# Optimization experiments

Hardware: AMD Instinct MI355X
Metric: run time of the kernel (lower is better)

Reference implementation:

```python
import jax, jax.numpy as jnp
import numpy as np

B, N, D, H = 4, 2048, 1024, 16
DH = D // H  # head dim = 64


def positional_encoding(n, dim):
    # Faithful vectorization of the numpy double loop in PositionalEncoding.
    i = jnp.arange(dim)
    even_i = (i % 2) == 0
    denom_i = 10000.0 ** (2.0 * jnp.where(even_i, i, i - 1).astype(jnp.float32) / dim)
    pos = jnp.arange(n, dtype=jnp.float32)[:, None]  # [n,1]
    base = jnp.where(even_i[None, :], jnp.sin(pos / denom_i), jnp.cos(pos / denom_i))  # [n,dim]
    p = jnp.arange(n)
    even_p = (p % 2) == 0
    denom_p = 10000.0 ** (2.0 * jnp.where(even_p, p, p - 1).astype(jnp.float32) / n)  # [n]
    j = jnp.arange(dim, dtype=jnp.float32)[None, :]  # [1,dim]
    mult = jnp.where(even_p[:, None], jnp.sin(j / denom_p[:, None]), jnp.cos(j / denom_p[:, None]))  # [n,dim]
    return base * mult


def setup_inputs() -> dict:
    key = jax.random.key(0)
    ks = jax.random.split(key, 4)
    s = 1.0 / np.sqrt(D)
    return {
        "data": jax.random.normal(ks[0], (B, N, D), dtype=jnp.float32),
        "Wq": jax.random.normal(ks[1], (D, D), dtype=jnp.float32) * s,
        "bq": jnp.zeros((D,), dtype=jnp.float32),
        "Wk": jax.random.normal(ks[2], (D, D), dtype=jnp.float32) * s,
        "bk": jnp.zeros((D,), dtype=jnp.float32),
        "Wv": jax.random.normal(ks[3], (D, D), dtype=jnp.float32) * s,
        "bv": jnp.zeros((D,), dtype=jnp.float32),
    }


def _split_heads(x):
    # tf.concat(tf.split(x, H, axis=-1), axis=0): head-major [H*B, N, DH]
    b, n, d = x.shape
    return x.reshape(b, n, H, DH).transpose(2, 0, 1, 3).reshape(H * b, n, DH)


def reference(data, Wq, bq, Wk, bk, Wv, bv):
    b, n, d = data.shape
    x = data + positional_encoding(n, d).astype(data.dtype)  # [B,N,D]
    q = _split_heads(x @ Wq + bq)  # [H*B,N,DH]
    k = _split_heads(x @ Wk + bk)
    v = _split_heads(x @ Wv + bv)
    # scale uses last dim of key AFTER split, i.e. head_dim
    scores = jnp.einsum('bqd,bkd->bqk', q, k) / jnp.sqrt(jnp.float32(DH))  # [H*B,N,N]
    w = jax.nn.softmax(scores, axis=-1)
    return jnp.einsum('bqk,bkd->bqd', w, v)  # [H*B,N,DH]
```

## Files before the change

kernel.cpp:

```cpp
#include <hip/hip_runtime.h>
#include <hip/hip_bf16.h>

#define BB 4
#define NN 2048
#define DD 1024
#define HH 16
#define DHH 64
#define HB (HH*BB)

typedef __bf16 bf16;
typedef __bf16 bf16x4v __attribute__((ext_vector_type(4)));
typedef __bf16 bf16x8 __attribute__((ext_vector_type(8)));
typedef float f32x4 __attribute__((ext_vector_type(4)));
typedef float f32x16 __attribute__((ext_vector_type(16)));
typedef unsigned u32x2 __attribute__((ext_vector_type(2)));

#if __has_builtin(__builtin_amdgcn_permlane32_swap)
#define HAVE_PLSWAP 1
#else
#define HAVE_PLSWAP 0
#endif

#define QSCALE 0.18033688011112042f

__device__ __forceinline__ void async16(const void* g, void* l) {
    __builtin_amdgcn_global_load_lds(
        (const __attribute__((address_space(1))) unsigned int*)g,
        (__attribute__((address_space(3))) unsigned int*)l, 16, 0, 0);
}

__device__ __forceinline__ unsigned pkbf(float a, float b) {
    union { bf16 h[2]; unsigned u; } x;
    x.h[0] = (bf16)a; x.h[1] = (bf16)b;
    return x.u;
}

__global__ void pe_add_kernel(const float* __restrict__ data, bf16* __restrict__ xb) {
    int t = blockIdx.x * blockDim.x + threadIdx.x;
    int base = t * 4;
    int row = base >> 10;
    int d0 = base & 1023;
    int n = row & (NN - 1);
    const float LOG2_10000 = 13.287712379549449f;
    int pn = n & ~1;
    float denom_p = __builtin_amdgcn_exp2f((2.0f * (float)pn / (float)NN) * LOG2_10000);
    bool even_p = (n & 1) == 0;
    float4 dv = *(const float4*)(data + base);
    float din[4] = {dv.x, dv.y, dv.z, dv.w};
    bf16x4v ov;
    #pragma unroll
    for (int u = 0; u < 4; ++u) {
        int d = d0 + u;
        int di = d & ~1;
        float denom_i = __builtin_amdgcn_exp2f((2.0f * (float)di / (float)DD) * LOG2_10000);
        float a = (float)n / denom_i;
        float basev = ((d & 1) == 0) ? __sinf(a) : __cosf(a);
        float bm = (float)d / denom_p;
        float mult = even_p ? __sinf(bm) : __cosf(bm);
        ov[u] = (bf16)(din[u] + basev * mult);
    }
    *(bf16x4v*)(xb + base) = ov;
}

__global__ void wtrans_kernel(const float* __restrict__ Wq, const float* __restrict__ Wk,
                              const float* __restrict__ Wv, bf16* __restrict__ Bw) {
    const float* W = (blockIdx.z == 0) ? Wq : (blockIdx.z == 1) ? Wk : Wv;
    bf16* Wt = Bw + (size_t)blockIdx.z * 1024 * 1024;
    __shared__ float s[32][33];
    int bx = blockIdx.x * 32;
    int by = blockIdx.y * 32;
    int tx = threadIdx.x, ty = threadIdx.y;
    #pragma unroll
    for (int i = 0; i < 32; i += 8)
        s[ty + i][tx] = W[(by + ty + i) * DD + bx + tx];
    __syncthreads();
    #pragma unroll
    for (int i = 0; i < 32; i += 8)
        Wt[(size_t)(bx + ty + i) * DD + by + tx] = (bf16)s[tx][ty + i];
}

__launch_bounds__(256)
__global__ void gemm_qkv_fused(const bf16* __restrict__ A,
                               const bf16* __restrict__ Bw,
                               const float* __restrict__ bq, const float* __restrict__ bk,
                               const float* __restrict__ bv,
                               bf16* __restrict__ Qs, bf16* __restrict__ Ks,
                               bf16* __restrict__ Vb) {
    __shared__ char smem[36864];
    int tid = threadIdx.x;
    int w = tid >> 6, lane = tid & 63, l32 = lane & 31, hi = lane >> 5;
    int bi = blockIdx.x;
    int bn = bi >> 6;
    int bm = (bi & 7) * 8 + ((bi >> 3) & 7);
    int m0 = bm * 128, n0 = bn * 128;
    int wm = (w & 1) * 64, wn = (w >> 1) * 64;

    int srow = tid >> 2;
    int g4 = (tid & 3) ^ (srow & 3);
    const bf16* aS0 = A + (size_t)(m0 + srow) * DD + g4 * 8;
    const bf16* aS1 = aS0 + (size_t)64 * DD;
    const bf16* bS0 = Bw + (size_t)(n0 + srow) * DD + g4 * 8;
    const bf16* bS1 = bS0 + (size_t)64 * DD;

    f32x16 acc[2][2];
    #pragma unroll
    for (int i = 0; i < 2; ++i)
        #pragma unroll
        for (int j = 0; j < 2; ++j)
            #pragma unroll
            for (int r = 0; r < 16; ++r) acc[i][j][r] = 0.f;

    async16(aS0, smem + w * 1024);
    async16(aS1, smem + 4096 + w * 1024);
    async16(bS0, smem + 8192 + w * 1024);
    async16(bS1, smem + 12288 + w * 1024);
    __syncthreads();

    for (int kk = 0; kk < DD; kk += 32) {
        char* buf  = smem + ((kk >> 5) & 1) * 16384;
        char* nbuf = smem + (((kk >> 5) & 1) ^ 1) * 16384;
        if (kk + 32 < DD) {
            async16(aS0 + kk + 32, nbuf + w * 1024);
            async16(aS1 + kk + 32, nbuf + 4096 + w * 1024);
            async16(bS0 + kk + 32, nbuf + 8192 + w * 1024);
            async16(bS1 + kk + 32, nbuf + 12288 + w * 1024);
        }
        const char* As = buf;
        const char* Bs = buf + 8192;
        bf16x8 af[2][2], bfr[2][2];
        #pragma unroll
        for (int mt = 0; mt < 2; ++mt) {
            int row = wm + mt * 32 + l32;
            #pragma unroll
            for (int kc = 0; kc < 2; ++kc)
                af[mt][kc] = *(const bf16x8*)(As + row * 64 + ((kc * 2 + hi) ^ (l32 & 3)) * 16);
        }
        #pragma unroll
        for (int nt = 0; nt < 2; ++nt) {
            int row = wn + nt * 32 + l32;
            #pragma unroll
            for (int kc = 0; kc < 2; ++kc)
                bfr[nt][kc] = *(const bf16x8*)(Bs + row * 64 + ((kc * 2 + hi) ^ (l32 & 3)) * 16);
        }
        #pragma unroll
        for (int mt = 0; mt < 2; ++mt)
            #pragma unroll
            for (int nt = 0; nt < 2; ++nt)
                #pragma unroll
                for (int kc = 0; kc < 2; ++kc)
                    acc[mt][nt] = __builtin_amdgcn_mfma_f32_32x32x16_bf16(
                        af[mt][kc], bfr[nt][kc], acc[mt][nt], 0, 0, 0);
        __syncthreads();
    }

    int mat = n0 >> 10;
    if (mat < 2) {
        const float* bias_p = (mat == 0) ? bq : bk;
        #pragma unroll
        for (int nt = 0; nt < 2; ++nt) {
            int ncol = (n0 + wn + nt * 32 + l32) & 1023;
            float bias = bias_p[ncol];
            int h = ncol >> 6, dh = ncol & 63;
            #pragma unroll
            for (int mt = 0; mt < 2; ++mt) {
                int rowbase = m0 + wm + mt * 32 + 4 * hi;
                #pragma unroll
                for (int m4 = 0; m4 < 4; ++m4) {
                    #pragma unroll
                    for (int rr = 0; rr < 4; ++rr) {
                        int mrow = rowbase + 8 * m4 + rr;
                        int b_ = mrow >> 11, nn_ = mrow & 2047;
                        int hbi = h * BB + b_;
                        float v = acc[mt][nt][m4 * 4 + rr] + bias;
                        if (mat == 0)
                            Qs[((size_t)hbi * NN + nn_) * DHH + dh] = (bf16)(v * QSCALE);
                        else
                            Ks[((size_t)hbi * NN + nn_) * DHH + dh] = (bf16)v;
                    }
                }
            }
        }
    } else {
        bf16* vl = (bf16*)smem;
        #pragma unroll
        for (int nt = 0; nt < 2; ++nt) {
            int ncol_l = wn + nt * 32 + l32;
            float bias = bv[(n0 + ncol_l) & 1023];
            #pragma unroll
            for (int mt = 0; mt < 2; ++mt) {
                int m_base = wm + mt * 32 + 4 * hi;
                #pragma unroll
                for (int m4 = 0; m4 < 4; ++m4) {
                    bf16x4v q;
                    #pragma unroll
                    for (int rr = 0; rr < 4; ++rr)
                        q[rr] = (bf16)(acc[mt][nt][m4 * 4 + rr] + bias);
                    *(bf16x4v*)(vl + ncol_l * 130 + m_base + 8 * m4) = q;
                }
            }
        }
        __syncthreads();
        int b_ = m0 >> 11, nn0 = m0 & 2047;
        #pragma unroll
        for (int p = 0; p < 2; ++p) {
            int ncol = p * 64 + (tid >> 2);
            int ncg = (n0 + ncol) & 1023;
            int h = ncg >> 6, dh = ncg & 63;
            bf16* dst = Vb + ((size_t)(h * BB + b_) * DHH + dh) * NN + nn0;
            #pragma unroll
            for (int i = 0; i < 4; ++i) {
                int eoff = ((tid & 3) + 4 * i) * 8;
                bf16x8 vv = *(const bf16x8*)(vl + ncol * 130 + eoff);
                *(bf16x8*)(dst + eoff) = vv;
            }
        }
    }
}

__launch_bounds__(256, 4)
__global__ void attn_kernel(const bf16* __restrict__ Qs,
                            const bf16* __restrict__ Ks,
                            const bf16* __restrict__ Vb,
                            float* __restrict__ out) {
    __shared__ char smem[32768];
    int tid = threadIdx.x;
    int w = tid >> 6, lane = tid & 63, l32 = lane & 31, hi = lane >> 5;
    int bi = blockIdx.x;
    int xcd = bi & 7, j = bi >> 3;
    int hb = xcd * 8 + (j & 7);
    int qb = j >> 3;
    int q0 = qb * 128 + w * 32;

    const bf16* qbase = Qs + ((size_t)hb * NN + q0 + l32) * DHH + hi * 8;
    bf16x8 qf[4];
    #pragma unroll
    for (int c = 0; c < 4; ++c)
        qf[c] = *(const bf16x8*)(qbase + c * 16);

    int srow = tid >> 3;
    int g8 = (tid & 7) ^ (srow & 7);
    const bf16* ksrc = Ks + ((size_t)hb * NN + srow) * DHH + g8 * 8;
    const bf16* vsrc = Vb + ((size_t)hb * DHH + srow) * NN + g8 * 8;

    f32x16 o[2], lacc;
    #pragma unroll
    for (int d = 0; d < 2; ++d)
        #pragma unroll
        for (int r = 0; r < 16; ++r) o[d][r] = 0.f;
    #pragma unroll
    for (int r = 0; r < 16; ++r) lacc[r] = 0.f;
    const bf16x8 onesf = {(bf16)1.f, (bf16)1.f, (bf16)1.f, (bf16)1.f,
                          (bf16)1.f, (bf16)1.f, (bf16)1.f, (bf16)1.f};

    async16(ksrc,            smem + w * 1024);
    async16(ksrc + 32 * 64,  smem + 4096 + w * 1024);
    async16(vsrc,            smem + 8192 + w * 1024);
    async16(vsrc + 32 * NN,  smem + 12288 + w * 1024);
    __syncthreads();

    for (int kt = 0; kt < NN; kt += 64) {
        char* buf  = smem + ((kt >> 6) & 1) * 16384;
        char* nbuf = smem + (((kt >> 6) & 1) ^ 1) * 16384;
        if (kt + 64 < NN) {
            async16(ksrc + (size_t)(kt + 64) * 64,      nbuf + w * 1024);
            async16(ksrc + (size_t)(kt + 96) * 64,      nbuf + 4096 + w * 1024);
            async16(vsrc + (kt + 64),                   nbuf + 8192 + w * 1024);
            async16(vsrc + (size_t)32 * NN + (kt + 64), nbuf + 12288 + w * 1024);
        }
        const char* ktile = buf;
        const char* vtile = buf + 8192;

        f32x16 sa[2];
        #pragma unroll
        for (int t = 0; t < 2; ++t) {
            #pragma unroll
            for (int r = 0; r < 16; ++r) sa[t][r] = 0.f;
            int row = t * 32 + l32;
            #pragma unroll
            for (int c = 0; c < 4; ++c) {
                bf16x8 kf = *(const bf16x8*)(ktile + row * 128 + ((c * 2 + hi) ^ (l32 & 7)) * 16);
                sa[t] = __builtin_amdgcn_mfma_f32_32x32x16_bf16(kf, qf[c], sa[t], 0, 0, 0);
            }
        }

        unsigned dw[2][4][2];
        #pragma unroll
        for (int t = 0; t < 2; ++t) {
            #pragma unroll
            for (int m4 = 0; m4 < 4; ++m4) {
                float p0 = __builtin_amdgcn_exp2f(sa[t][m4 * 4 + 0]);
                float p1 = __builtin_amdgcn_exp2f(sa[t][m4 * 4 + 1]);
                float p2 = __builtin_amdgcn_exp2f(sa[t][m4 * 4 + 2]);
                float p3 = __builtin_amdgcn_exp2f(sa[t][m4 * 4 + 3]);
                dw[t][m4][0] = pkbf(p0, p1);
                dw[t][m4][1] = pkbf(p2, p3);
            }
        }

        #pragma unroll
        for (int c = 0; c < 4; ++c) {
            int t = c >> 1, mlo = (c & 1) * 2;
            unsigned a0 = dw[t][mlo][0],     a1 = dw[t][mlo][1];
            unsigned b0 = dw[t][mlo + 1][0], b1 = dw[t][mlo + 1][1];
            union { unsigned u[4]; bf16x8 v; } pu;
#if HAVE_PLSWAP
            u32x2 r0 = __builtin_amdgcn_permlane32_swap(a0, b0, false, false);
            u32x2 r1 = __builtin_amdgcn_permlane32_swap(a1, b1, false, false);
            pu.u[0] = r0.x; pu.u[1] = r1.x; pu.u[2] = r0.y; pu.u[3] = r1.y;
#else
            unsigned own0 = hi ? b0 : a0, own1 = hi ? b1 : a1;
            unsigned snd0 = hi ? a0 : b0, snd1 = hi ? a1 : b1;
            unsigned rcv0 = __shfl_xor(snd0, 32, 64);
            unsigned rcv1 = __shfl_xor(snd1, 32, 64);
            pu.u[0] = hi ? rcv0 : own0;
            pu.u[1] = hi ? rcv1 : own1;
            pu.u[2] = hi ? own0 : rcv0;
            pu.u[3] = hi ? own1 : rcv1;
#endif
            #pragma unroll
            for (int d = 0; d < 2; ++d) {
                int row = d * 32 + l32;
                bf16x8 vf = *(const bf16x8*)(vtile + row * 128 + ((c * 2 + hi) ^ (l32 & 7)) * 16);
                o[d] = __builtin_amdgcn_mfma_f32_32x32x16_bf16(vf, pu.v, o[d], 0, 0, 0);
            }
            lacc = __builtin_amdgcn_mfma_f32_32x32x16_bf16(onesf, pu.v, lacc, 0, 0, 0);
        }
        __syncthreads();
    }

    float inv = 1.0f / lacc[0];
    float* ob = out + ((size_t)hb * NN + q0 + l32) * DHH + 4 * hi;
    #pragma unroll
    for (int d = 0; d < 2; ++d) {
        #pragma unroll
        for (int m4 = 0; m4 < 4; ++m4) {
            f32x4 vv;
            vv[0] = o[d][m4 * 4 + 0] * inv;
            vv[1] = o[d][m4 * 4 + 1] * inv;
            vv[2] = o[d][m4 * 4 + 2] * inv;
            vv[3] = o[d][m4 * 4 + 3] * inv;
            *(f32x4*)(ob + d * 32 + 8 * m4) = vv;
        }
    }
}

extern "C" void kernel_launch(void* const* d_in, const int* in_sizes, int n_in,
                              void* d_out, int out_size, void* d_ws, size_t ws_size,
                              hipStream_t stream) {
    const float* data = (const float*)d_in[0];
    const float* Wq   = (const float*)d_in[1];
    const float* bq   = (const float*)d_in[2];
    const float* Wk   = (const float*)d_in[3];
    const float* bk   = (const float*)d_in[4];
    const float* Wv   = (const float*)d_in[5];
    const float* bv   = (const float*)d_in[6];
    float* out = (float*)d_out;

    char* ws = (char*)d_ws;
    bf16* xb = (bf16*)ws; ws += (size_t)8192 * 1024 * 2;
    bf16* Bw = (bf16*)ws; ws += (size_t)3072 * 1024 * 2;
    bf16* Qs = (bf16*)ws; ws += (size_t)HB * NN * DHH * 2;
    bf16* Ks = (bf16*)ws; ws += (size_t)HB * NN * DHH * 2;
    bf16* Vb = (bf16*)ws; ws += (size_t)HB * NN * DHH * 2;

    pe_add_kernel<<<8192, 256, 0, stream>>>(data, xb);
    dim3 tb(32, 8), tg(32, 32, 3);
    wtrans_kernel<<<tg, tb, 0, stream>>>(Wq, Wk, Wv, Bw);
    gemm_qkv_fused<<<1536, 256, 0, stream>>>(xb, Bw, bq, bk, bv, Qs, Ks, Vb);
    attn_kernel<<<1024, 256, 0, stream>>>(Qs, Ks, Vb, out);
}
```

Before: 260.4 us.

## Split attention waves across query and key halves, reduce partial outputs in LDS

```diff
diff --git a/kernel.cpp b/kernel.cpp
--- a/kernel.cpp
+++ b/kernel.cpp
@@ -217,40 +217,43 @@
     }
 }
 
-__launch_bounds__(256, 4)
+__launch_bounds__(256, 3)
 __global__ void attn_kernel(const bf16* __restrict__ Qs,
                             const bf16* __restrict__ Ks,
                             const bf16* __restrict__ Vb,
                             float* __restrict__ out) {
-    __shared__ char smem[32768];
+    __shared__ char smem[33280];
     int tid = threadIdx.x;
     int w = tid >> 6, lane = tid & 63, l32 = lane & 31, hi = lane >> 5;
+    int qh = w & 1, kh = w >> 1;
     int bi = blockIdx.x;
-    int xcd = bi & 7, j = bi >> 3;
-    int hb = xcd * 8 + (j & 7);
-    int qb = j >> 3;
-    int q0 = qb * 128 + w * 32;
-
-    const bf16* qbase = Qs + ((size_t)hb * NN + q0 + l32) * DHH + hi * 8;
-    bf16x8 qf[4];
-    #pragma unroll
-    for (int c = 0; c < 4; ++c)
-        qf[c] = *(const bf16x8*)(qbase + c * 16);
+    int xcd = bi & 7, jj = bi >> 3;
+    int hb = xcd * 8 + (jj & 7);
+    int qb = jj >> 3;
+    int q0 = qb * 128;
+
+    bf16x8 qf[2][4];
+    #pragma unroll
+    for (int qs = 0; qs < 2; ++qs) {
+        const bf16* qbase = Qs + ((size_t)hb * NN + q0 + qh * 64 + qs * 32 + l32) * DHH + hi * 8;
+        #pragma unroll
+        for (int c = 0; c < 4; ++c)
+            qf[qs][c] = *(const bf16x8*)(qbase + c * 16);
+    }
 
     int srow = tid >> 3;
     int g8 = (tid & 7) ^ (srow & 7);
     const bf16* ksrc = Ks + ((size_t)hb * NN + srow) * DHH + g8 * 8;
     const bf16* vsrc = Vb + ((size_t)hb * DHH + srow) * NN + g8 * 8;
 
-    f32x16 o[2], lacc;
-    #pragma unroll
-    for (int d = 0; d < 2; ++d)
-        #pragma unroll
-        for (int r = 0; r < 16; ++r) o[d][r] = 0.f;
-    #pragma unroll
-    for (int r = 0; r < 16; ++r) lacc[r] = 0.f;
-    const bf16x8 onesf = {(bf16)1.f, (bf16)1.f, (bf16)1.f, (bf16)1.f,
-                          (bf16)1.f, (bf16)1.f, (bf16)1.f, (bf16)1.f};
+    f32x16 o[2][2];
+    #pragma unroll
+    for (int qs = 0; qs < 2; ++qs)
+        #pragma unroll
+        for (int d = 0; d < 2; ++d)
+            #pragma unroll
+            for (int r = 0; r < 16; ++r) o[qs][d][r] = 0.f;
+    float ts[2] = {0.f, 0.f};
 
     async16(ksrc,            smem + w * 1024);
     async16(ksrc + 32 * 64,  smem + 4096 + w * 1024);
@@ -270,77 +273,135 @@
         const char* ktile = buf;
         const char* vtile = buf + 8192;
 
+        bf16x8 kf[4];
+        int krow = kh * 32 + l32;
+        #pragma unroll
+        for (int c = 0; c < 4; ++c)
+            kf[c] = *(const bf16x8*)(ktile + krow * 128 + ((c * 2 + hi) ^ (l32 & 7)) * 16);
+
         f32x16 sa[2];
         #pragma unroll
-        for (int t = 0; t < 2; ++t) {
-            #pragma unroll
-            for (int r = 0; r < 16; ++r) sa[t][r] = 0.f;
-            int row = t * 32 + l32;
-            #pragma unroll
-            for (int c = 0; c < 4; ++c) {
-                bf16x8 kf = *(const bf16x8*)(ktile + row * 128 + ((c * 2 + hi) ^ (l32 & 7)) * 16);
-                sa[t] = __builtin_amdgcn_mfma_f32_32x32x16_bf16(kf, qf[c], sa[t], 0, 0, 0);
-            }
+        for (int qs = 0; qs < 2; ++qs) {
+            #pragma unroll
+            for (int r = 0; r < 16; ++r) sa[qs][r] = 0.f;
+            #pragma unroll
+            for (int c = 0; c < 4; ++c)
+                sa[qs] = __builtin_amdgcn_mfma_f32_32x32x16_bf16(kf[c], qf[qs][c], sa[qs], 0, 0, 0);
         }
 
         unsigned dw[2][4][2];
         #pragma unroll
-        for (int t = 0; t < 2; ++t) {
+        for (int qs = 0; qs < 2; ++qs) {
+            float t0 = 0.f;
             #pragma unroll
             for (int m4 = 0; m4 < 4; ++m4) {
-                float p0 = __builtin_amdgcn_exp2f(sa[t][m4 * 4 + 0]);
-                float p1 = __builtin_amdgcn_exp2f(sa[t][m4 * 4 + 1]);
-                float p2 = __builtin_amdgcn_exp2f(sa[t][m4 * 4 + 2]);
-                float p3 = __builtin_amdgcn_exp2f(sa[t][m4 * 4 + 3]);
-                dw[t][m4][0] = pkbf(p0, p1);
-                dw[t][m4][1] = pkbf(p2, p3);
-            }
-        }
-
-        #pragma unroll
-        for (int c = 0; c < 4; ++c) {
-            int t = c >> 1, mlo = (c & 1) * 2;
-            unsigned a0 = dw[t][mlo][0],     a1 = dw[t][mlo][1];
-            unsigned b0 = dw[t][mlo + 1][0], b1 = dw[t][mlo + 1][1];
-            union { unsigned u[4]; bf16x8 v; } pu;
+                float p0 = __builtin_amdgcn_exp2f(sa[qs][m4 * 4 + 0]);
+                float p1 = __builtin_amdgcn_exp2f(sa[qs][m4 * 4 + 1]);
+                float p2 = __builtin_amdgcn_exp2f(sa[qs][m4 * 4 + 2]);
+                float p3 = __builtin_amdgcn_exp2f(sa[qs][m4 * 4 + 3]);
+                t0 += (p0 + p1) + (p2 + p3);
+                dw[qs][m4][0] = pkbf(p0, p1);
+                dw[qs][m4][1] = pkbf(p2, p3);
+            }
+            ts[qs] += t0;
+        }
+
+        #pragma unroll
+        for (int kc = 0; kc < 2; ++kc) {
+            bf16x8 vf[2];
+            #pragma unroll
+            for (int d = 0; d < 2; ++d) {
+                int vrow = d * 32 + l32;
+                vf[d] = *(const bf16x8*)(vtile + vrow * 128 +
+                                         ((kh * 4 + kc * 2 + hi) ^ (l32 & 7)) * 16);
+            }
+            #pragma unroll
+            for (int qs = 0; qs < 2; ++qs) {
+                int mlo = kc * 2;
+                unsigned a0 = dw[qs][mlo][0],     a1 = dw[qs][mlo][1];
+                unsigned b0 = dw[qs][mlo + 1][0], b1 = dw[qs][mlo + 1][1];
+                union { unsigned u[4]; bf16x8 v; } pu;
 #if HAVE_PLSWAP
-            u32x2 r0 = __builtin_amdgcn_permlane32_swap(a0, b0, false, false);
-            u32x2 r1 = __builtin_amdgcn_permlane32_swap(a1, b1, false, false);
-            pu.u[0] = r0.x; pu.u[1] = r1.x; pu.u[2] = r0.y; pu.u[3] = r1.y;
+                u32x2 r0 = __builtin_amdgcn_permlane32_swap(a0, b0, false, false);
+                u32x2 r1 = __builtin_amdgcn_permlane32_swap(a1, b1, false, false);
+                pu.u[0] = r0.x; pu.u[1] = r1.x; pu.u[2] = r0.y; pu.u[3] = r1.y;
 #else
-            unsigned own0 = hi ? b0 : a0, own1 = hi ? b1 : a1;
-            unsigned snd0 = hi ? a0 : b0, snd1 = hi ? a1 : b1;
-            unsigned rcv0 = __shfl_xor(snd0, 32, 64);
-            unsigned rcv1 = __shfl_xor(snd1, 32, 64);
-            pu.u[0] = hi ? rcv0 : own0;
-            pu.u[1] = hi ? rcv1 : own1;
-            pu.u[2] = hi ? own0 : rcv0;
-            pu.u[3] = hi ? own1 : rcv1;
+                unsigned own0 = hi ? b0 : a0, own1 = hi ? b1 : a1;
+                unsigned snd0 = hi ? a0 : b0, snd1 = hi ? a1 : b1;
+                unsigned rcv0 = __shfl_xor(snd0, 32, 64);
+                unsigned rcv1 = __shfl_xor(snd1, 32, 64);
+                pu.u[0] = hi ? rcv0 : own0;
+                pu.u[1] = hi ? rcv1 : own1;
+                pu.u[2] = hi ? own0 : rcv0;
+                pu.u[3] = hi ? own1 : rcv1;
 #endif
-            #pragma unroll
-            for (int d = 0; d < 2; ++d) {
-                int row = d * 32 + l32;
-                bf16x8 vf = *(const bf16x8*)(vtile + row * 128 + ((c * 2 + hi) ^ (l32 & 7)) * 16);
-                o[d] = __builtin_amdgcn_mfma_f32_32x32x16_bf16(vf, pu.v, o[d], 0, 0, 0);
-            }
-            lacc = __builtin_amdgcn_mfma_f32_32x32x16_bf16(onesf, pu.v, lacc, 0, 0, 0);
+                #pragma unroll
+                for (int d = 0; d < 2; ++d)
+                    o[qs][d] = __builtin_amdgcn_mfma_f32_32x32x16_bf16(vf[d], pu.v, o[qs][d], 0, 0, 0);
+            }
         }
         __syncthreads();
     }
 
-    float inv = 1.0f / lacc[0];
-    float* ob = out + ((size_t)hb * NN + q0 + l32) * DHH + 4 * hi;
-    #pragma unroll
-    for (int d = 0; d < 2; ++d) {
-        #pragma unroll
-        for (int m4 = 0; m4 < 4; ++m4) {
-            f32x4 vv;
-            vv[0] = o[d][m4 * 4 + 0] * inv;
-            vv[1] = o[d][m4 * 4 + 1] * inv;
-            vv[2] = o[d][m4 * 4 + 2] * inv;
-            vv[3] = o[d][m4 * 4 + 3] * inv;
-            *(f32x4*)(ob + d * 32 + 8 * m4) = vv;
-        }
+    float* Osm = (float*)smem;
+    float* Ls  = (float*)(smem + 32768);
+    float tsq[2];
+    #pragma unroll
+    for (int qs = 0; qs < 2; ++qs)
+        tsq[qs] = ts[qs] + __shfl_xor(ts[qs], 32, 64);
+
+    if (kh == 0) {
+        #pragma unroll
+        for (int qs = 0; qs < 2; ++qs) {
+            int q_l = qh * 64 + qs * 32 + l32;
+            #pragma unroll
+            for (int d = 0; d < 2; ++d)
+                #pragma unroll
+                for (int m4 = 0; m4 < 4; ++m4) {
+                    int ci = d * 8 + m4 * 2 + hi;
+                    int pc = ci ^ (q_l & 15);
+                    f32x4 v;
+                    v[0] = o[qs][d][m4 * 4 + 0];
+                    v[1] = o[qs][d][m4 * 4 + 1];
+                    v[2] = o[qs][d][m4 * 4 + 2];
+                    v[3] = o[qs][d][m4 * 4 + 3];
+                    *(f32x4*)(Osm + q_l * 64 + pc * 4) = v;
+                }
+            if (!hi) Ls[q_l] = tsq[qs];
+        }
+    }
+    __syncthreads();
+    if (kh == 1) {
+        #pragma unroll
+        for (int qs = 0; qs < 2; ++qs) {
+            int q_l = qh * 64 + qs * 32 + l32;
+            #pragma unroll
+            for (int d = 0; d < 2; ++d)
+                #pragma unroll
+                for (int m4 = 0; m4 < 4; ++m4) {
+                    int ci = d * 8 + m4 * 2 + hi;
+                    int pc = ci ^ (q_l & 15);
+                    f32x4 v = *(const f32x4*)(Osm + q_l * 64 + pc * 4);
+                    v[0] += o[qs][d][m4 * 4 + 0];
+                    v[1] += o[qs][d][m4 * 4 + 1];
+                    v[2] += o[qs][d][m4 * 4 + 2];
+                    v[3] += o[qs][d][m4 * 4 + 3];
+                    *(f32x4*)(Osm + q_l * 64 + pc * 4) = v;
+                }
+            if (!hi) Ls[q_l] += tsq[qs];
+        }
+    }
+    __syncthreads();
+    float* outb = out + ((size_t)hb * NN + q0) * DHH;
+    #pragma unroll
+    for (int i = 0; i < 8; ++i) {
+        int g = tid + 256 * i;
+        int q_l = g >> 4, ci = g & 15;
+        int pc = ci ^ (q_l & 15);
+        float inv = 1.0f / Ls[q_l];
+        f32x4 v = *(const f32x4*)(Osm + q_l * 64 + pc * 4);
+        v *= inv;
+        *(f32x4*)(outb + g * 4) = v;
     }
 }
 
```

New measurement: 256.0 us. Within noise of the previous version (-1.7%).
